# Kernel tuning notes

Measured on AMD Instinct MI355X. Metric: run time of the kernel, lower is better.

The kernel has to match this reference:

```python
import jax, jax.numpy as jnp
import numpy as np


def log_g(x):
    # torch: where(x>=0, log(relu(x)+0.5), -softplus(-x))
    return jnp.where(x >= 0, jnp.log(jnp.maximum(x, 0.0) + 0.5), -jax.nn.softplus(-x))


def parallel_scan_log(log_coeffs, log_values):
    # log_coeffs: [B, T, H], log_values: [B, T+1, H]
    a_star = jnp.cumsum(log_coeffs, axis=1)
    a_star = jnp.pad(a_star, ((0, 0), (1, 0), (0, 0)))  # [B, T+1, H]
    log_h0_plus_b_star = jax.lax.cumlogsumexp(log_values - a_star, axis=1)
    return jnp.exp(a_star + log_h0_plus_b_star)


def setup_inputs() -> dict:
    key = jax.random.key(0)
    B, T, I, H = 8, 4096, 1024, 1024
    k1, k2, k3, k4, k5, k6 = jax.random.split(key, 6)
    scale = 1.0 / np.sqrt(I)
    return {
        "x": jax.random.normal(k1, (B, T, I), dtype=jnp.float32),
        "h_0": jax.random.normal(k2, (B, H), dtype=jnp.float32),
        "W_z": jax.random.uniform(k3, (H, I), jnp.float32, -scale, scale),
        "b_z": jax.random.uniform(k4, (H,), jnp.float32, -scale, scale),
        "W_h": jax.random.uniform(k5, (H, I), jnp.float32, -scale, scale),
        "b_h": jax.random.uniform(k6, (H,), jnp.float32, -scale, scale),
    }


def reference(x, h_0, W_z, b_z, W_h, b_h):
    T = x.shape[1]
    k = jnp.einsum("bti,hi->bth", x, W_z) + b_z          # linear_z(x)
    log_z = -jax.nn.softplus(-k)
    log_coeffs = -jax.nn.softplus(k)
    log_h_0 = log_g(h_0)[:, None, :]                      # [B, 1, H]
    log_tilde_h = log_g(jnp.einsum("bti,hi->bth", x, W_h) + b_h)
    log_values = jnp.concatenate([log_h_0, log_z + log_tilde_h], axis=1)
    h = parallel_scan_log(log_coeffs, log_values)         # [B, T+1, H]
    return h[:, -T:, :]
```

## Files before the change

kernel.cpp:

```cpp
#include <hip/hip_runtime.h>
#include <hip/hip_bf16.h>
#include <math.h>

typedef _Float16 half8_t __attribute__((ext_vector_type(8)));
typedef _Float16 half4_t __attribute__((ext_vector_type(4)));
typedef float    floatx4 __attribute__((ext_vector_type(4)));

#define GLOAD16(gp, lp) __builtin_amdgcn_global_load_lds( \
    (const __attribute__((address_space(1))) void*)(gp),  \
    (__attribute__((address_space(3))) void*)(lp), 16, 0, 0)

static constexpr int Bc  = 8;
static constexpr int Tc  = 4096;
static constexpr int Ic  = 1024;
static constexpr int Hc  = 1024;
static constexpr int Mc  = Bc * Tc;
static constexpr int NC2 = 128;
static constexpr int L2c = Tc / NC2;

__global__ void cvt_kernel(const float* __restrict__ in, _Float16* __restrict__ out, long n)
{
    long i = ((long)blockIdx.x * blockDim.x + threadIdx.x) * 4;
    long stride = (long)gridDim.x * blockDim.x * 4;
    for (; i < n; i += stride) {
        float4 v = *reinterpret_cast<const float4*>(in + i);
        half4_t h;
        h[0] = (_Float16)v.x; h[1] = (_Float16)v.y;
        h[2] = (_Float16)v.z; h[3] = (_Float16)v.w;
        *reinterpret_cast<half4_t*>(out + i) = h;
    }
}

__global__ __launch_bounds__(512) void dual_gemm_f16(
    const _Float16* __restrict__ A,
    const _Float16* __restrict__ Wz,
    const _Float16* __restrict__ Wh,
    const float* __restrict__ bz,
    const float* __restrict__ bh,
    _Float16* __restrict__ k16,
    _Float16* __restrict__ p16)
{
    constexpr int BK = 32, K = Ic, N = Hc, NSTEP = K / BK;
    __shared__ __align__(16) _Float16 sA [2][128 * BK];
    __shared__ __align__(16) _Float16 sBz[2][128 * BK];
    __shared__ __align__(16) _Float16 sBh[2][128 * BK];

    const int bid     = blockIdx.x;
    const int logical = (bid & 7) * 256 + (bid >> 3);
    const int n0 = (logical & 7) * 128;
    const int m0 = (logical >> 3) * 128;

    const int tid  = threadIdx.x;
    const int lane = tid & 63;
    const int wave = tid >> 6;
    const int zsel = wave >> 2;
    const int wr = (wave >> 1) & 1, wc = wave & 1;

    const int srow = tid >> 2;
    const int schk = (tid & 3) * 8;
    const int soff = srow * BK + schk;
    const _Float16* gA  = A  + (size_t)(m0 + srow) * K + schk;
    const _Float16* gBz = Wz + (size_t)(n0 + srow) * K + schk;
    const _Float16* gBh = Wh + (size_t)(n0 + srow) * K + schk;

    const int lrow = lane & 15;
    const int kch  = (lane >> 4) * 8;
    const _Float16* sBsel = zsel ? &sBh[0][0] : &sBz[0][0];
    const int aoff = (wr * 64 + lrow) * BK + kch;
    const int boff = (wc * 64 + lrow) * BK + kch;

    floatx4 acc[4][4];
#pragma unroll
    for (int m = 0; m < 4; m++)
#pragma unroll
        for (int n = 0; n < 4; n++) acc[m][n] = (floatx4){0.f, 0.f, 0.f, 0.f};

    GLOAD16(gA,  &sA [0][soff]);
    GLOAD16(gBz, &sBz[0][soff]);
    GLOAD16(gBh, &sBh[0][soff]);
    __syncthreads();

    int buf = 0;
    for (int ki = 0; ki < NSTEP; ki++) {
        if (ki + 1 < NSTEP) {
            const int kt = (ki + 1) * BK;
            GLOAD16(gA  + kt, &sA [buf ^ 1][soff]);
            GLOAD16(gBz + kt, &sBz[buf ^ 1][soff]);
            GLOAD16(gBh + kt, &sBh[buf ^ 1][soff]);
        }
        const half8_t* rA = (const half8_t*)&sA[buf][aoff];
        const half8_t* rB = (const half8_t*)(sBsel + (size_t)buf * (128 * BK) + boff);
        half8_t af[4], bf[4];
#pragma unroll
        for (int m = 0; m < 4; m++) af[m] = rA[m * 64];
#pragma unroll
        for (int n = 0; n < 4; n++) bf[n] = rB[n * 64];
#pragma unroll
        for (int m = 0; m < 4; m++)
#pragma unroll
            for (int n = 0; n < 4; n++)
                acc[m][n] = __builtin_amdgcn_mfma_f32_16x16x32_f16(af[m], bf[n], acc[m][n], 0, 0, 0);
        __syncthreads();
        buf ^= 1;
    }

    _Float16* C = zsel ? p16 : k16;
    const float* bias = zsel ? bh : bz;
    const int r0 = (lane >> 4) * 4;
#pragma unroll
    for (int n = 0; n < 4; n++) {
        const int col = n0 + wc * 64 + n * 16 + lrow;
        const float bv = bias[col];
#pragma unroll
        for (int m = 0; m < 4; m++) {
            const int row = m0 + wr * 64 + m * 16 + r0;
#pragma unroll
            for (int r = 0; r < 4; r++)
                C[(size_t)(row + r) * N + col] = (_Float16)(acc[m][n][r] + bv);
        }
    }
}

__device__ __forceinline__ float sigm(float x) { return 1.0f / (1.0f + __expf(-x)); }
__device__ __forceinline__ float g_fn(float x) { return x >= 0.0f ? x + 0.5f : sigm(x); }
__device__ __forceinline__ void fv_from_kp(float kk, float pp, float& f, float& v)
{
    float ek = __expf(kk);
    f = 1.0f / (1.0f + ek);
    float z = 1.0f - f;
    v = z * g_fn(pp);
}

__global__ __launch_bounds__(128) void scanA(const _Float16* __restrict__ k16,
                                             const _Float16* __restrict__ p16,
                                             float* __restrict__ Fb, float* __restrict__ Sb)
{
    const int b = blockIdx.y, c = blockIdx.x;
    const int h0 = threadIdx.x * 8;
    size_t base = ((size_t)b * Tc + (size_t)c * L2c) * Hc + h0;
    float F[8], S[8];
#pragma unroll
    for (int j = 0; j < 8; j++) { F[j] = 1.0f; S[j] = 0.0f; }
    for (int t = 0; t < L2c; t++) {
        half8_t k8 = *reinterpret_cast<const half8_t*>(k16 + base + (size_t)t * Hc);
        half8_t p8 = *reinterpret_cast<const half8_t*>(p16 + base + (size_t)t * Hc);
#pragma unroll
        for (int j = 0; j < 8; j++) {
            float f, v; fv_from_kp((float)k8[j], (float)p8[j], f, v);
            S[j] = fmaf(f, S[j], v);
            F[j] *= f;
        }
    }
    size_t ci = ((size_t)b * NC2 + c) * Hc + h0;
#pragma unroll
    for (int j = 0; j < 8; j++) { Fb[ci + j] = F[j]; Sb[ci + j] = S[j]; }
}

__global__ void scanB(const float* __restrict__ h0p, const float* __restrict__ Fb,
                      const float* __restrict__ Sb, float* __restrict__ Cin)
{
    const int idx = blockIdx.x * blockDim.x + threadIdx.x;
    const int b = idx >> 10, h = idx & 1023;
    float carry = g_fn(h0p[(size_t)b * Hc + h]);
    for (int c = 0; c < NC2; c++) {
        size_t ci = ((size_t)b * NC2 + c) * Hc + h;
        Cin[ci] = carry;
        carry = fmaf(Fb[ci], carry, Sb[ci]);
    }
}

__global__ __launch_bounds__(128) void scanC(const _Float16* __restrict__ k16,
                                             const _Float16* __restrict__ p16,
                                             const float* __restrict__ Cin,
                                             float* __restrict__ out)
{
    const int b = blockIdx.y, c = blockIdx.x;
    const int h0 = threadIdx.x * 8;
    size_t base = ((size_t)b * Tc + (size_t)c * L2c) * Hc + h0;
    size_t ci = ((size_t)b * NC2 + c) * Hc + h0;
    float hr[8];
#pragma unroll
    for (int j = 0; j < 8; j++) hr[j] = Cin[ci + j];
    for (int t = 0; t < L2c; t++) {
        half8_t k8 = *reinterpret_cast<const half8_t*>(k16 + base + (size_t)t * Hc);
        half8_t p8 = *reinterpret_cast<const half8_t*>(p16 + base + (size_t)t * Hc);
#pragma unroll
        for (int j = 0; j < 8; j++) {
            float f, v; fv_from_kp((float)k8[j], (float)p8[j], f, v);
            hr[j] = fmaf(f, hr[j], v);
        }
        float4 o0 = make_float4(hr[0], hr[1], hr[2], hr[3]);
        float4 o1 = make_float4(hr[4], hr[5], hr[6], hr[7]);
        *reinterpret_cast<float4*>(out + base + (size_t)t * Hc)     = o0;
        *reinterpret_cast<float4*>(out + base + (size_t)t * Hc + 4) = o1;
    }
}

extern "C" void kernel_launch(void* const* d_in, const int* in_sizes, int n_in,
                              void* d_out, int out_size, void* d_ws, size_t ws_size,
                              hipStream_t stream)
{
    const float* x  = (const float*)d_in[0];
    const float* h0 = (const float*)d_in[1];
    const float* Wz = (const float*)d_in[2];
    const float* bz = (const float*)d_in[3];
    const float* Wh = (const float*)d_in[4];
    const float* bh = (const float*)d_in[5];
    float* out = (float*)d_out;

    char* ws = (char*)d_ws;
    _Float16* x16  = (_Float16*)ws;
    _Float16* w16z = (_Float16*)(ws + 67108864ULL);
    _Float16* w16h = (_Float16*)(ws + 69206016ULL);
    _Float16* k16  = (_Float16*)(ws + 71303168ULL);
    _Float16* p16  = (_Float16*)(ws + 138412032ULL);
    float* Fb  = (float*)(ws + 205520896ULL);
    float* Sb  = (float*)(ws + 209715200ULL);
    float* Cin = (float*)(ws + 213909504ULL);

    cvt_kernel<<<2048, 256, 0, stream>>>(x,  x16,  (long)Mc * Ic);
    cvt_kernel<<<256,  256, 0, stream>>>(Wz, w16z, (long)Hc * Ic);
    cvt_kernel<<<256,  256, 0, stream>>>(Wh, w16h, (long)Hc * Ic);

    dual_gemm_f16<<<2048, 512, 0, stream>>>(x16, w16z, w16h, bz, bh, k16, p16);

    dim3 sgrid(NC2, Bc);
    scanA<<<sgrid, 128, 0, stream>>>(k16, p16, Fb, Sb);
    scanB<<<32, 256, 0, stream>>>(h0, Fb, Sb, Cin);
    scanC<<<sgrid, 128, 0, stream>>>(k16, p16, Cin, out);
}
```

Measured before the change: 504.1 us.

## Fuse chunk-scan reduction into GEMM epilogue and merge conversion kernels

The per-chunk (F, S) scan reduction that scanA computed by re-reading k16/p16 now happens in the GEMM epilogue. The h-half waves stage g(p) in shared memory, and the z-half waves combine 16-row chunks with cross-lane shuffles. This removes a full pass over the two fp16 intermediates. The three fp32-to-fp16 conversion launches are merged into one, the chunk count goes to 256 with a transposed Fb/Sb/Cin layout for vectorized scanB, and Cin reuses the x16 workspace. The epilogue is now longer and has an extra barrier, and scanC reads Cin with a strided access pattern.

```diff
diff --git a/kernel.cpp b/kernel.cpp
--- a/kernel.cpp
+++ b/kernel.cpp
@@ -15,19 +15,34 @@
 static constexpr int Ic  = 1024;
 static constexpr int Hc  = 1024;
 static constexpr int Mc  = Bc * Tc;
-static constexpr int NC2 = 128;
-static constexpr int L2c = Tc / NC2;
-
-__global__ void cvt_kernel(const float* __restrict__ in, _Float16* __restrict__ out, long n)
-{
-    long i = ((long)blockIdx.x * blockDim.x + threadIdx.x) * 4;
-    long stride = (long)gridDim.x * blockDim.x * 4;
+static constexpr int NCc = 256;
+static constexpr int Lc  = Tc / NCc;
+
+__device__ __forceinline__ float sigm(float x) { return 1.0f / (1.0f + __expf(-x)); }
+__device__ __forceinline__ float g_fn(float x) { return x >= 0.0f ? x + 0.5f : sigm(x); }
+__device__ __forceinline__ void fv_from_kp(float kk, float pp, float& f, float& v)
+{
+    float ek = __expf(kk);
+    f = 1.0f / (1.0f + ek);
+    v = (1.0f - f) * g_fn(pp);
+}
+
+__global__ __launch_bounds__(256) void cvt_all(
+    const float* __restrict__ x,  const float* __restrict__ Wz, const float* __restrict__ Wh,
+    _Float16* __restrict__ x16, _Float16* __restrict__ w16z, _Float16* __restrict__ w16h)
+{
+    const float* src; _Float16* dst; long n, bid, nb;
+    if (blockIdx.x < 2048)      { src = x;  dst = x16;  n = (long)Mc * Ic; bid = blockIdx.x;        nb = 2048; }
+    else if (blockIdx.x < 2112) { src = Wz; dst = w16z; n = (long)Hc * Ic; bid = blockIdx.x - 2048; nb = 64; }
+    else                        { src = Wh; dst = w16h; n = (long)Hc * Ic; bid = blockIdx.x - 2112; nb = 64; }
+    long i = (bid * 256 + threadIdx.x) * 4;
+    long stride = nb * 256 * 4;
     for (; i < n; i += stride) {
-        float4 v = *reinterpret_cast<const float4*>(in + i);
+        float4 v = *reinterpret_cast<const float4*>(src + i);
         half4_t h;
         h[0] = (_Float16)v.x; h[1] = (_Float16)v.y;
         h[2] = (_Float16)v.z; h[3] = (_Float16)v.w;
-        *reinterpret_cast<half4_t*>(out + i) = h;
+        *reinterpret_cast<half4_t*>(dst + i) = h;
     }
 }
 
@@ -38,12 +53,15 @@
     const float* __restrict__ bz,
     const float* __restrict__ bh,
     _Float16* __restrict__ k16,
-    _Float16* __restrict__ p16)
+    _Float16* __restrict__ p16,
+    float* __restrict__ Fb,
+    float* __restrict__ Sb)
 {
     constexpr int BK = 32, K = Ic, N = Hc, NSTEP = K / BK;
-    __shared__ __align__(16) _Float16 sA [2][128 * BK];
-    __shared__ __align__(16) _Float16 sBz[2][128 * BK];
-    __shared__ __align__(16) _Float16 sBh[2][128 * BK];
+    __shared__ __align__(16) _Float16 smem[24576];
+    _Float16* sA  = smem;
+    _Float16* sBz = smem + 8192;
+    _Float16* sBh = smem + 16384;
 
     const int bid     = blockIdx.x;
     const int logical = (bid & 7) * 256 + (bid >> 3);
@@ -65,7 +83,7 @@
 
     const int lrow = lane & 15;
     const int kch  = (lane >> 4) * 8;
-    const _Float16* sBsel = zsel ? &sBh[0][0] : &sBz[0][0];
+    const _Float16* sBsel = zsel ? sBh : sBz;
     const int aoff = (wr * 64 + lrow) * BK + kch;
     const int boff = (wc * 64 + lrow) * BK + kch;
 
@@ -75,21 +93,22 @@
 #pragma unroll
         for (int n = 0; n < 4; n++) acc[m][n] = (floatx4){0.f, 0.f, 0.f, 0.f};
 
-    GLOAD16(gA,  &sA [0][soff]);
-    GLOAD16(gBz, &sBz[0][soff]);
-    GLOAD16(gBh, &sBh[0][soff]);
+    GLOAD16(gA,  &sA [soff]);
+    GLOAD16(gBz, &sBz[soff]);
+    GLOAD16(gBh, &sBh[soff]);
     __syncthreads();
 
     int buf = 0;
     for (int ki = 0; ki < NSTEP; ki++) {
         if (ki + 1 < NSTEP) {
             const int kt = (ki + 1) * BK;
-            GLOAD16(gA  + kt, &sA [buf ^ 1][soff]);
-            GLOAD16(gBz + kt, &sBz[buf ^ 1][soff]);
-            GLOAD16(gBh + kt, &sBh[buf ^ 1][soff]);
-        }
-        const half8_t* rA = (const half8_t*)&sA[buf][aoff];
-        const half8_t* rB = (const half8_t*)(sBsel + (size_t)buf * (128 * BK) + boff);
+            const int po = (buf ^ 1) * 4096 + soff;
+            GLOAD16(gA  + kt, &sA [po]);
+            GLOAD16(gBz + kt, &sBz[po]);
+            GLOAD16(gBh + kt, &sBh[po]);
+        }
+        const half8_t* rA = (const half8_t*)&sA[buf * 4096 + aoff];
+        const half8_t* rB = (const half8_t*)(sBsel + buf * 4096 + boff);
         half8_t af[4], bf[4];
 #pragma unroll
         for (int m = 0; m < 4; m++) af[m] = rA[m * 64];
@@ -104,68 +123,82 @@
         buf ^= 1;
     }
 
-    _Float16* C = zsel ? p16 : k16;
-    const float* bias = zsel ? bh : bz;
     const int r0 = (lane >> 4) * 4;
-#pragma unroll
-    for (int n = 0; n < 4; n++) {
-        const int col = n0 + wc * 64 + n * 16 + lrow;
-        const float bv = bias[col];
-#pragma unroll
-        for (int m = 0; m < 4; m++) {
-            const int row = m0 + wr * 64 + m * 16 + r0;
-#pragma unroll
-            for (int r = 0; r < 4; r++)
-                C[(size_t)(row + r) * N + col] = (_Float16)(acc[m][n][r] + bv);
-        }
-    }
-}
-
-__device__ __forceinline__ float sigm(float x) { return 1.0f / (1.0f + __expf(-x)); }
-__device__ __forceinline__ float g_fn(float x) { return x >= 0.0f ? x + 0.5f : sigm(x); }
-__device__ __forceinline__ void fv_from_kp(float kk, float pp, float& f, float& v)
-{
-    float ek = __expf(kk);
-    f = 1.0f / (1.0f + ek);
-    float z = 1.0f - f;
-    v = z * g_fn(pp);
-}
-
-__global__ __launch_bounds__(128) void scanA(const _Float16* __restrict__ k16,
-                                             const _Float16* __restrict__ p16,
-                                             float* __restrict__ Fb, float* __restrict__ Sb)
-{
-    const int b = blockIdx.y, c = blockIdx.x;
-    const int h0 = threadIdx.x * 8;
-    size_t base = ((size_t)b * Tc + (size_t)c * L2c) * Hc + h0;
-    float F[8], S[8];
-#pragma unroll
-    for (int j = 0; j < 8; j++) { F[j] = 1.0f; S[j] = 0.0f; }
-    for (int t = 0; t < L2c; t++) {
-        half8_t k8 = *reinterpret_cast<const half8_t*>(k16 + base + (size_t)t * Hc);
-        half8_t p8 = *reinterpret_cast<const half8_t*>(p16 + base + (size_t)t * Hc);
-#pragma unroll
-        for (int j = 0; j < 8; j++) {
-            float f, v; fv_from_kp((float)k8[j], (float)p8[j], f, v);
-            S[j] = fmaf(f, S[j], v);
-            F[j] *= f;
-        }
-    }
-    size_t ci = ((size_t)b * NC2 + c) * Hc + h0;
-#pragma unroll
-    for (int j = 0; j < 8; j++) { Fb[ci + j] = F[j]; Sb[ci + j] = S[j]; }
-}
-
-__global__ void scanB(const float* __restrict__ h0p, const float* __restrict__ Fb,
-                      const float* __restrict__ Sb, float* __restrict__ Cin)
-{
-    const int idx = blockIdx.x * blockDim.x + threadIdx.x;
+    _Float16* gpL = smem;
+
+    if (zsel) {
+#pragma unroll
+        for (int n = 0; n < 4; n++) {
+            const int colL = wc * 64 + n * 16 + lrow;
+            const float bv = bh[n0 + colL];
+#pragma unroll
+            for (int m = 0; m < 4; m++) {
+                const int rowL = wr * 64 + m * 16 + r0;
+#pragma unroll
+                for (int r = 0; r < 4; r++) {
+                    _Float16 ph = (_Float16)(acc[m][n][r] + bv);
+                    p16[(size_t)(m0 + rowL + r) * N + (n0 + colL)] = ph;
+                    gpL[(rowL + r) * 128 + colL] = (_Float16)g_fn((float)ph);
+                }
+            }
+        }
+    }
+    __syncthreads();
+    if (!zsel) {
+        const int b    = m0 >> 12;
+        const int trow = m0 & 4095;
+#pragma unroll
+        for (int n = 0; n < 4; n++) {
+            const int colL = wc * 64 + n * 16 + lrow;
+            const int col  = n0 + colL;
+            const float bv = bz[col];
+#pragma unroll
+            for (int m = 0; m < 4; m++) {
+                const int rowL = wr * 64 + m * 16 + r0;
+                float Fl = 1.0f, Sl = 0.0f;
+#pragma unroll
+                for (int r = 0; r < 4; r++) {
+                    _Float16 kh = (_Float16)(acc[m][n][r] + bv);
+                    k16[(size_t)(m0 + rowL + r) * N + col] = kh;
+                    float f = 1.0f / (1.0f + __expf((float)kh));
+                    float v = (1.0f - f) * (float)gpL[(rowL + r) * 128 + colL];
+                    Sl = fmaf(f, Sl, v);
+                    Fl *= f;
+                }
+                float Fp = __shfl_xor(Fl, 16), Sp = __shfl_xor(Sl, 16);
+                Sl = (lane & 16) ? fmaf(Sp, Fl, Sl) : fmaf(Sl, Fp, Sp);
+                Fl *= Fp;
+                Fp = __shfl_xor(Fl, 32); Sp = __shfl_xor(Sl, 32);
+                Sl = (lane & 32) ? fmaf(Sp, Fl, Sl) : fmaf(Sl, Fp, Sp);
+                Fl *= Fp;
+                if (lane < 16) {
+                    const int c = (trow + wr * 64 + m * 16) >> 4;
+                    const size_t idx = ((size_t)b * Hc + col) * NCc + c;
+                    Fb[idx] = Fl; Sb[idx] = Sl;
+                }
+            }
+        }
+    }
+}
+
+__global__ __launch_bounds__(128) void scanB(const float* __restrict__ h0p,
+                                             const float* __restrict__ Fb,
+                                             const float* __restrict__ Sb,
+                                             float* __restrict__ Cin)
+{
+    const int idx = blockIdx.x * 128 + threadIdx.x;
     const int b = idx >> 10, h = idx & 1023;
     float carry = g_fn(h0p[(size_t)b * Hc + h]);
-    for (int c = 0; c < NC2; c++) {
-        size_t ci = ((size_t)b * NC2 + c) * Hc + h;
-        Cin[ci] = carry;
-        carry = fmaf(Fb[ci], carry, Sb[ci]);
+    const size_t base = ((size_t)b * Hc + h) * NCc;
+    for (int c = 0; c < NCc; c += 4) {
+        float4 F4 = *reinterpret_cast<const float4*>(Fb + base + c);
+        float4 S4 = *reinterpret_cast<const float4*>(Sb + base + c);
+        float4 C4;
+        C4.x = carry; carry = fmaf(F4.x, carry, S4.x);
+        C4.y = carry; carry = fmaf(F4.y, carry, S4.y);
+        C4.z = carry; carry = fmaf(F4.z, carry, S4.z);
+        C4.w = carry; carry = fmaf(F4.w, carry, S4.w);
+        *reinterpret_cast<float4*>(Cin + base + c) = C4;
     }
 }
 
@@ -176,12 +209,12 @@
 {
     const int b = blockIdx.y, c = blockIdx.x;
     const int h0 = threadIdx.x * 8;
-    size_t base = ((size_t)b * Tc + (size_t)c * L2c) * Hc + h0;
-    size_t ci = ((size_t)b * NC2 + c) * Hc + h0;
+    size_t base = ((size_t)b * Tc + (size_t)c * Lc) * Hc + h0;
     float hr[8];
 #pragma unroll
-    for (int j = 0; j < 8; j++) hr[j] = Cin[ci + j];
-    for (int t = 0; t < L2c; t++) {
+    for (int j = 0; j < 8; j++)
+        hr[j] = Cin[((size_t)b * Hc + h0 + j) * NCc + c];
+    for (int t = 0; t < Lc; t++) {
         half8_t k8 = *reinterpret_cast<const half8_t*>(k16 + base + (size_t)t * Hc);
         half8_t p8 = *reinterpret_cast<const half8_t*>(p16 + base + (size_t)t * Hc);
 #pragma unroll
@@ -189,10 +222,8 @@
             float f, v; fv_from_kp((float)k8[j], (float)p8[j], f, v);
             hr[j] = fmaf(f, hr[j], v);
         }
-        float4 o0 = make_float4(hr[0], hr[1], hr[2], hr[3]);
-        float4 o1 = make_float4(hr[4], hr[5], hr[6], hr[7]);
-        *reinterpret_cast<float4*>(out + base + (size_t)t * Hc)     = o0;
-        *reinterpret_cast<float4*>(out + base + (size_t)t * Hc + 4) = o1;
+        *reinterpret_cast<float4*>(out + base + (size_t)t * Hc)     = make_float4(hr[0], hr[1], hr[2], hr[3]);
+        *reinterpret_cast<float4*>(out + base + (size_t)t * Hc + 4) = make_float4(hr[4], hr[5], hr[6], hr[7]);
     }
 }
 
@@ -215,17 +246,15 @@
     _Float16* k16  = (_Float16*)(ws + 71303168ULL);
     _Float16* p16  = (_Float16*)(ws + 138412032ULL);
     float* Fb  = (float*)(ws + 205520896ULL);
-    float* Sb  = (float*)(ws + 209715200ULL);
-    float* Cin = (float*)(ws + 213909504ULL);
-
-    cvt_kernel<<<2048, 256, 0, stream>>>(x,  x16,  (long)Mc * Ic);
-    cvt_kernel<<<256,  256, 0, stream>>>(Wz, w16z, (long)Hc * Ic);
-    cvt_kernel<<<256,  256, 0, stream>>>(Wh, w16h, (long)Hc * Ic);
-
-    dual_gemm_f16<<<2048, 512, 0, stream>>>(x16, w16z, w16h, bz, bh, k16, p16);
-
-    dim3 sgrid(NC2, Bc);
-    scanA<<<sgrid, 128, 0, stream>>>(k16, p16, Fb, Sb);
-    scanB<<<32, 256, 0, stream>>>(h0, Fb, Sb, Cin);
-    scanC<<<sgrid, 128, 0, stream>>>(k16, p16, Cin, out);
-}
+    float* Sb  = (float*)(ws + 213909504ULL);
+    float* Cin = (float*)ws;
+
+    cvt_all<<<2176, 256, 0, stream>>>(x, Wz, Wh, x16, w16z, w16h);
+
+    dual_gemm_f16<<<2048, 512, 0, stream>>>(x16, w16z, w16h, bz, bh, k16, p16, Fb, Sb);
+
+    scanB<<<64, 128, 0, stream>>>(h0, Fb, Sb, Cin);
+
+    dim3 cgrid(NCc, Bc);
+    scanC<<<cgrid, 128, 0, stream>>>(k16, p16, Cin, out);
+}
```

After: 531.6 us. 1.05x slower.
